# Kernel optimization log

Measured on AMD Instinct MI355X. Metric: run time of the kernel, lower is better.

The kernel has to match this reference:

```python
import jax, jax.numpy as jnp
import numpy as np

B, T, D_MODEL = 2, 2048, 2048
N_HEADS, N_KV, HEAD_DIM = 16, 8, 128
ROPE_BASE = 10000.0
LAMBDA_INIT = 0.2  # 0.8 - 0.6*exp(-0.3*0), layer_depth=0


def rms_norm(x):
    eps = jnp.finfo(x.dtype).eps
    return x * jax.lax.rsqrt(jnp.mean(x * x, axis=-1, keepdims=True) + eps)


def rope_cos_sin(seq_len, dim):
    inv_freq = 1.0 / (ROPE_BASE ** (np.arange(0, dim, 2, dtype=np.float32) / dim))
    t = np.arange(seq_len, dtype=np.float32)
    freqs = np.outer(t, inv_freq)  # [T, dim/2]
    # original caches cos/sin in bfloat16
    cos = jnp.asarray(np.cos(freqs)).astype(jnp.bfloat16).astype(jnp.float32)
    sin = jnp.asarray(np.sin(freqs)).astype(jnp.bfloat16).astype(jnp.float32)
    return cos[None, :, None, :], sin[None, :, None, :]


def apply_rotary(x, cos, sin):
    d = x.shape[-1] // 2
    x1, x2 = x[..., :d], x[..., d:]
    return jnp.concatenate([x1 * cos + x2 * sin, -x1 * sin + x2 * cos], axis=-1)


def causal_attn(q, k, v):
    # q: [B,T,H,Dq], k: [B,S,H,Dq], v: [B,S,H,Dv]
    scale = 1.0 / np.sqrt(q.shape[-1]).astype(np.float32)
    s = jnp.einsum('bthd,bshd->bhts', q, k) * scale
    mask = jnp.tril(jnp.ones((q.shape[1], k.shape[1]), dtype=bool))
    s = jnp.where(mask, s, -jnp.inf)
    p = jax.nn.softmax(s, axis=-1)
    return jnp.einsum('bhts,bshe->bthe', p, v)


def diff_attention(x, Wq, Wk, Wv, lambda_q1, lambda_k1, lambda_q2, lambda_k2, softmax_scaler):
    b, t, _ = x.shape
    q = (x @ Wq.T).reshape(b, t, N_HEADS, HEAD_DIM)
    k = (x @ Wk.T).reshape(b, t, N_KV, HEAD_DIM)
    v = (x @ Wv.T).reshape(b, t, N_KV // 2, 2 * HEAD_DIM)
    cos, sin = rope_cos_sin(t, HEAD_DIM)
    q, k = rms_norm(q), rms_norm(k)
    q, k = apply_rotary(q, cos, sin), apply_rotary(k, cos, sin)
    k = k.reshape(b, t, 2, N_KV // 2, HEAD_DIM)
    k1, k2 = k[:, :, 0], k[:, :, 1]
    # scalable softmax: q *= scaler_h * log(position)
    pos = jnp.arange(1, t + 1, dtype=jnp.float32).reshape(1, t, 1, 1)
    q = softmax_scaler.reshape(1, 1, -1, 1) * jnp.log(pos) * q
    q = q.reshape(b, t, 2, N_HEADS // 2, HEAD_DIM)
    q1, q2 = q[:, :, 0], q[:, :, 1]
    rep = N_HEADS // N_KV  # GQA repeat
    k1 = jnp.repeat(k1, rep, axis=2)
    k2 = jnp.repeat(k2, rep, axis=2)
    vr = jnp.repeat(v, rep, axis=2)
    y1 = causal_attn(q1, k1, vr)
    y2 = causal_attn(q2, k2, vr)
    lam1 = jnp.exp(jnp.sum(lambda_q1 * lambda_k1))
    lam2 = jnp.exp(jnp.sum(lambda_q2 * lambda_k2))
    lam = lam1 - lam2 + LAMBDA_INIT
    return y1 - lam * y2  # [B,T,N_HEADS//2, 2*HEAD_DIM]


def setup_inputs() -> dict:
    key = jax.random.key(0)
    ks = jax.random.split(key, 8)
    return {
        'x': jax.random.normal(ks[0], (B, T, D_MODEL), dtype=jnp.float32),
        'Wq': jax.random.normal(ks[1], (N_HEADS * HEAD_DIM, D_MODEL), dtype=jnp.float32) * 0.02,
        'Wk': jax.random.normal(ks[2], (N_KV * HEAD_DIM, D_MODEL), dtype=jnp.float32) * 0.02,
        'Wv': jax.random.normal(ks[3], (N_KV * HEAD_DIM, D_MODEL), dtype=jnp.float32) * 0.02,
        'lambda_q1': jax.random.normal(ks[4], (HEAD_DIM // 2,), dtype=jnp.float32) * 0.1,
        'lambda_k1': jax.random.normal(ks[5], (HEAD_DIM // 2,), dtype=jnp.float32) * 0.1,
        'lambda_q2': jax.random.normal(ks[6], (HEAD_DIM // 2,), dtype=jnp.float32) * 0.1,
        'lambda_k2': jax.random.normal(ks[7], (HEAD_DIM // 2,), dtype=jnp.float32) * 0.1,
        'softmax_scaler': jnp.ones((N_HEADS,), dtype=jnp.float32),
    }


def reference(x, Wq, Wk, Wv, lambda_q1, lambda_k1, lambda_q2, lambda_k2, softmax_scaler):
    return diff_attention(x, Wq, Wk, Wv, lambda_q1, lambda_k1, lambda_q2, lambda_k2, softmax_scaler)
```

## Files before the change

kernel.cpp:

```cpp
#include <hip/hip_runtime.h>

#define T_SEQ 2048
#define DMODEL 2048
#define BSZ 2
#define MROWS (BSZ * T_SEQ)
#define NQKV 4096
#define NEG_BIG (-1e30f)

typedef __attribute__((ext_vector_type(8))) _Float16 half8;
typedef __attribute__((ext_vector_type(4))) _Float16 half4;
typedef __attribute__((ext_vector_type(4))) float f32x4;

typedef const __attribute__((address_space(1))) unsigned int* gas_ptr;
typedef __attribute__((address_space(3))) unsigned int* las_ptr;
#define GLD16(g, l) __builtin_amdgcn_global_load_lds((gas_ptr)(g), (las_ptr)(l), 16, 0, 0)

__device__ __forceinline__ unsigned short f2bf(float f) {
  unsigned u = __float_as_uint(f);
  unsigned r = (u + 0x7fffu + ((u >> 16) & 1u)) >> 16;
  return (unsigned short)r;
}
__device__ __forceinline__ float bf2f(unsigned short h) {
  return __uint_as_float(((unsigned)h) << 16);
}

__global__ void build_rope(float* __restrict__ cosT, float* __restrict__ sinT) {
  int t = blockIdx.x;
  int i = threadIdx.x;
  float inv = (float)pow(10000.0, -((double)(2 * i)) / 128.0);
  float fr = (float)t * inv;
  cosT[t * 64 + i] = bf2f(f2bf(cosf(fr)));
  sinT[t * 64 + i] = bf2f(f2bf(sinf(fr)));
}

__global__ __launch_bounds__(256) void cvt_x(const float* __restrict__ x,
                                             _Float16* __restrict__ xh) {
  size_t o = ((size_t)blockIdx.x * 256 + threadIdx.x) * 8;
  float4 v0 = *(const float4*)(x + o);
  float4 v1 = *(const float4*)(x + o + 4);
  half8 r;
  r[0] = (_Float16)v0.x; r[1] = (_Float16)v0.y; r[2] = (_Float16)v0.z; r[3] = (_Float16)v0.w;
  r[4] = (_Float16)v1.x; r[5] = (_Float16)v1.y; r[6] = (_Float16)v1.z; r[7] = (_Float16)v1.w;
  *(half8*)(xh + o) = r;
}

__global__ __launch_bounds__(256) void cvt_w(const float* __restrict__ Wq,
                                             const float* __restrict__ Wk,
                                             const float* __restrict__ Wv,
                                             _Float16* __restrict__ wh) {
  size_t o = ((size_t)blockIdx.x * 256 + threadIdx.x) * 8;
  int row = (int)(o >> 11), col = (int)(o & 2047);
  const float* src = (row < 2048) ? (Wq + (size_t)row * 2048)
                    : (row < 3072) ? (Wk + (size_t)(row - 2048) * 2048)
                                   : (Wv + (size_t)(row - 3072) * 2048);
  float4 v0 = *(const float4*)(src + col);
  float4 v1 = *(const float4*)(src + col + 4);
  half8 r;
  r[0] = (_Float16)v0.x; r[1] = (_Float16)v0.y; r[2] = (_Float16)v0.z; r[3] = (_Float16)v0.w;
  r[4] = (_Float16)v1.x; r[5] = (_Float16)v1.y; r[6] = (_Float16)v1.z; r[7] = (_Float16)v1.w;
  *(half8*)(wh + o) = r;
}

__global__ __launch_bounds__(256) void gemm_nt(const _Float16* __restrict__ A,
                                               const _Float16* __restrict__ Bw,
                                               _Float16* __restrict__ C) {
  const int K = DMODEL, N = NQKV;
  __shared__ _Float16 At[128 * 40];
  __shared__ _Float16 Bt[128 * 40];
  int tid = threadIdx.x;
  int lane = tid & 63, w = tid >> 6;
  int wm = w >> 1, wn = w & 1;
  int l15 = lane & 15, quad = lane >> 4;
  int bm = blockIdx.y, bn = blockIdx.x;

  f32x4 acc[4][4];
#pragma unroll
  for (int i = 0; i < 4; i++)
#pragma unroll
    for (int j = 0; j < 4; j++) acc[i][j] = (f32x4){0.f, 0.f, 0.f, 0.f};

  for (int k0 = 0; k0 < K; k0 += 32) {
    __syncthreads();
#pragma unroll
    for (int i = 0; i < 2; i++) {
      int idx = i * 256 + tid;
      int r = idx >> 2, c = idx & 3;
      *(half8*)&At[r * 40 + c * 8] =
          *(const half8*)(A + (size_t)(bm * 128 + r) * K + k0 + c * 8);
      *(half8*)&Bt[r * 40 + c * 8] =
          *(const half8*)(Bw + (size_t)(bn * 128 + r) * K + k0 + c * 8);
    }
    __syncthreads();
    half8 af[4], bfr[4];
#pragma unroll
    for (int i = 0; i < 4; i++)
      af[i] = *(const half8*)&At[(wm * 64 + i * 16 + l15) * 40 + quad * 8];
#pragma unroll
    for (int j = 0; j < 4; j++)
      bfr[j] = *(const half8*)&Bt[(wn * 64 + j * 16 + l15) * 40 + quad * 8];
#pragma unroll
    for (int i = 0; i < 4; i++)
#pragma unroll
      for (int j = 0; j < 4; j++)
        acc[i][j] = __builtin_amdgcn_mfma_f32_16x16x32_f16(af[i], bfr[j], acc[i][j], 0, 0, 0);
  }
#pragma unroll
  for (int i = 0; i < 4; i++)
#pragma unroll
    for (int j = 0; j < 4; j++)
#pragma unroll
      for (int r = 0; r < 4; r++) {
        int row = bm * 128 + wm * 64 + i * 16 + quad * 4 + r;
        int col = bn * 128 + wn * 64 + j * 16 + l15;
        C[(size_t)row * N + col] = (_Float16)acc[i][j][r];
      }
}

__global__ __launch_bounds__(128) void postproc(_Float16* __restrict__ qkv,
                                                const float* __restrict__ cosT,
                                                const float* __restrict__ sinT,
                                                _Float16* __restrict__ kp) {
  int t = blockIdx.x, h = blockIdx.y, b = blockIdx.z;
  int d = threadIdx.x;
  int col = (h < 16) ? (h * 128 + d) : (2048 + (h - 16) * 128 + d);
  size_t idx = ((size_t)(b * T_SEQ + t)) * NQKV + col;
  float v = (float)qkv[idx];
  float ss = v * v;
#pragma unroll
  for (int m = 1; m < 64; m <<= 1) ss += __shfl_xor(ss, m, 64);
  __shared__ float sred[2];
  __shared__ float xs[128];
  if ((threadIdx.x & 63) == 0) sred[threadIdx.x >> 6] = ss;
  __syncthreads();
  float total = sred[0] + sred[1];
  float rn = rsqrtf(total * (1.0f / 128.0f) + 1.1920929e-7f);
  float xn = v * rn;
  xs[d] = xn;
  __syncthreads();
  float o;
  if (d < 64) {
    float c = cosT[t * 64 + d], s = sinT[t * 64 + d];
    o = xn * c + xs[d + 64] * s;
  } else {
    float c = cosT[t * 64 + d - 64], s = sinT[t * 64 + d - 64];
    o = -xs[d - 64] * s + xn * c;
  }
  if (h < 16)
    qkv[idx] = (_Float16)o;
  else
    kp[(((size_t)(b * 8 + (h - 16))) * T_SEQ + t) * 128 + d] = (_Float16)o;
}

__global__ void transpose_v(const _Float16* __restrict__ qkv,
                            _Float16* __restrict__ vt) {
  __shared__ _Float16 tile[32][33];
  int t0 = blockIdx.x * 32, d0 = blockIdx.y * 32;
  int bz = blockIdx.z;
  int b = bz >> 2, vh = bz & 3;
  int tx = threadIdx.x, ty = threadIdx.y;
#pragma unroll
  for (int i = 0; i < 4; i++) {
    int t = t0 + ty + i * 8;
    tile[ty + i * 8][tx] = qkv[((size_t)(b * T_SEQ + t)) * NQKV + 3072 + vh * 256 + d0 + tx];
  }
  __syncthreads();
#pragma unroll
  for (int i = 0; i < 4; i++) {
    int d = d0 + ty + i * 8;
    vt[(((size_t)(b * 4 + vh)) * 256 + d) * T_SEQ + t0 + tx] = tile[tx][ty + i * 8];
  }
}

__global__ __launch_bounds__(256) void attn(const _Float16* __restrict__ qkv,
                                            const _Float16* __restrict__ kp,
                                            const _Float16* __restrict__ vt,
                                            const float* __restrict__ scaler,
                                            float* __restrict__ y1out,
                                            _Float16* __restrict__ y2out) {
  __shared__ __align__(16) char Ks[2][64 * 256];
  __shared__ __align__(16) char Vs[2][128 * 128];
  __shared__ _Float16 Pt[4 * 16 * 72];

  int tid = threadIdx.x, lane = tid & 63, w = tid >> 6;
  int l15 = lane & 15, quad = lane >> 4;
  int bx = blockIdx.x, hh = blockIdx.y, z = blockIdx.z;
  int b = z >> 1, br = z & 1;
  int qh = br * 8 + hh;
  int kh = br * 4 + (hh >> 1);
  int vh = hh >> 1;

  const char* kbase_b = (const char*)(kp + ((size_t)(b * 8 + kh)) * T_SEQ * 128);
  const char* vbase_b = (const char*)(vt + ((size_t)(b * 4 + vh)) * 256 * T_SEQ);
  _Float16* pw = &Pt[w * 16 * 72];
  float sc = scaler[qh] * 0.08838834764831844f;

  int krow_l = lane >> 4;
  int kpc    = (lane & 15) << 4;
  int vrow_l = lane >> 3;
  int vpc    = (lane & 7) << 4;

  auto stageK = [&](int kt1) {
    int ksr = kt1 * 64;
    char* dstb = Ks[kt1 & 1];
#pragma unroll
    for (int c2 = 0; c2 < 4; c2++) {
      int c = w * 4 + c2;
      int row = c * 4 + krow_l;
      const char* src = kbase_b + (((size_t)(ksr + row)) << 8) + (kpc ^ ((row & 7) << 4));
      GLD16(src, dstb + (c << 10));
    }
  };
  auto stageV = [&](int kt1) {
    int ksb = kt1 * 128;
#pragma unroll
    for (int h = 0; h < 2; h++)
#pragma unroll
      for (int c2 = 0; c2 < 4; c2++) {
        int c = w * 4 + c2;
        int d = h * 128 + c * 8 + vrow_l;
        const char* src = vbase_b + (size_t)d * (T_SEQ * 2) + ksb + (vpc ^ (vrow_l << 4));
        GLD16(src, Vs[h] + (c << 10));
      }
  };

  for (int half = 0; half < 2; half++) {
    int qt = half ? (31 - bx) : bx;
    int t0 = qt * 64;
    int tg = t0 + w * 16 + l15;

    const _Float16* qbase = qkv + ((size_t)(b * T_SEQ + tg)) * NQKV + qh * 128;
    half8 qf[4];
#pragma unroll
    for (int kc = 0; kc < 4; kc++)
      qf[kc] = *(const half8*)(qbase + kc * 32 + quad * 8);

    stageK(0);
    stageV(0);
    __builtin_amdgcn_sched_barrier(0);

    float mrow = NEG_BIG, lrow = 0.f;
    float rowscale = sc * logf((float)(tg + 1));
    f32x4 acc[16];
#pragma unroll
    for (int nb = 0; nb < 16; nb++) acc[nb] = (f32x4){0.f, 0.f, 0.f, 0.f};

    for (int kt = 0; kt <= qt; kt++) {
      int ks = kt * 64;
      bool notlast = (kt < qt);

      asm volatile("s_waitcnt vmcnt(8)" ::: "memory");
      __builtin_amdgcn_s_barrier();
      __builtin_amdgcn_sched_barrier(0);
      if (notlast) stageK(kt + 1);

      const char* kbuf = Ks[kt & 1];
      f32x4 sv[4];
#pragma unroll
      for (int j = 0; j < 4; j++) {
        int row = j * 16 + l15;
        int sw = (row & 7) << 4;
        const char* kr = kbuf + (row << 8);
        half8 kf0 = *(const half8*)(kr + (((quad << 4) + 0) ^ sw));
        half8 kf1 = *(const half8*)(kr + (((quad << 4) + 64) ^ sw));
        half8 kf2 = *(const half8*)(kr + (((quad << 4) + 128) ^ sw));
        half8 kf3 = *(const half8*)(kr + (((quad << 4) + 192) ^ sw));
        f32x4 a = (f32x4){0.f, 0.f, 0.f, 0.f};
        a = __builtin_amdgcn_mfma_f32_16x16x32_f16(kf0, qf[0], a, 0, 0, 0);
        a = __builtin_amdgcn_mfma_f32_16x16x32_f16(kf1, qf[1], a, 0, 0, 0);
        a = __builtin_amdgcn_mfma_f32_16x16x32_f16(kf2, qf[2], a, 0, 0, 0);
        a = __builtin_amdgcn_mfma_f32_16x16x32_f16(kf3, qf[3], a, 0, 0, 0);
        sv[j] = a;
      }

      bool diag = (kt == qt);
      float s_r[16];
      float mx = NEG_BIG;
#pragma unroll
      for (int j = 0; j < 4; j++)
#pragma unroll
        for (int r = 0; r < 4; r++) {
          float s = sv[j][r] * rowscale;
          if (diag) {
            int kg = ks + j * 16 + quad * 4 + r;
            if (kg > tg) s = NEG_BIG;
          }
          s_r[j * 4 + r] = s;
          mx = fmaxf(mx, s);
        }
      mx = fmaxf(mx, __shfl_xor(mx, 16, 64));
      mx = fmaxf(mx, __shfl_xor(mx, 32, 64));
      float mnew = fmaxf(mrow, mx);
      float alpha = __expf(mrow - mnew);
      float p[16];
      float rs = 0.f;
#pragma unroll
      for (int i = 0; i < 16; i++) {
        p[i] = __expf(s_r[i] - mnew);
        rs += p[i];
      }
      rs += __shfl_xor(rs, 16, 64);
      rs += __shfl_xor(rs, 32, 64);
      lrow = lrow * alpha + rs;
      mrow = mnew;
      float at[4];
#pragma unroll
      for (int r = 0; r < 4; r++) at[r] = __shfl(alpha, quad * 20 + r, 64);
#pragma unroll
      for (int nb = 0; nb < 16; nb++)
#pragma unroll
        for (int r = 0; r < 4; r++) acc[nb][r] *= at[r];

#pragma unroll
      for (int j = 0; j < 4; j++) {
        half4 pk;
        pk[0] = (_Float16)p[j * 4 + 0];
        pk[1] = (_Float16)p[j * 4 + 1];
        pk[2] = (_Float16)p[j * 4 + 2];
        pk[3] = (_Float16)p[j * 4 + 3];
        *(half4*)&pw[l15 * 72 + j * 16 + quad * 4] = pk;
      }
      half8 pf0 = *(const half8*)&pw[l15 * 72 + quad * 8];
      half8 pf1 = *(const half8*)&pw[l15 * 72 + 32 + quad * 8];

      if (notlast)
        asm volatile("s_waitcnt vmcnt(4)" ::: "memory");
      else
        asm volatile("s_waitcnt vmcnt(0)" ::: "memory");
      __builtin_amdgcn_s_barrier();
      __builtin_amdgcn_sched_barrier(0);

#pragma unroll
      for (int h = 0; h < 2; h++) {
#pragma unroll
        for (int nbl = 0; nbl < 8; nbl++) {
          int row = nbl * 16 + l15;
          int sw = (row & 7) << 4;
          const char* vr = Vs[h] + (row << 7);
          half8 vf0 = *(const half8*)(vr + (((quad << 4) + 0) ^ sw));
          half8 vf1 = *(const half8*)(vr + (((quad << 4) + 64) ^ sw));
          int nb = h * 8 + nbl;
          acc[nb] = __builtin_amdgcn_mfma_f32_16x16x32_f16(pf0, vf0, acc[nb], 0, 0, 0);
          acc[nb] = __builtin_amdgcn_mfma_f32_16x16x32_f16(pf1, vf1, acc[nb], 0, 0, 0);
        }
      }

      asm volatile("s_waitcnt lgkmcnt(0)" ::: "memory");
      __builtin_amdgcn_s_barrier();
      __builtin_amdgcn_sched_barrier(0);
      if (notlast) stageV(kt + 1);
    }

    float linv = 1.0f / lrow;
    float lt[4];
#pragma unroll
    for (int r = 0; r < 4; r++) lt[r] = __shfl(linv, quad * 20 + r, 64);
#pragma unroll
    for (int r = 0; r < 4; r++) {
      int tr = t0 + w * 16 + quad * 4 + r;
      size_t base = ((size_t)(b * T_SEQ + tr)) * 2048 + hh * 256;
      if (br) {
#pragma unroll
        for (int nb = 0; nb < 16; nb++)
          y2out[base + nb * 16 + l15] = (_Float16)(acc[nb][r] * lt[r]);
      } else {
#pragma unroll
        for (int nb = 0; nb < 16; nb++)
          y1out[base + nb * 16 + l15] = acc[nb][r] * lt[r];
      }
    }
  }
}

__global__ __launch_bounds__(256) void combine(float* __restrict__ out,
                                               const _Float16* __restrict__ y2,
                                               const float* __restrict__ lq1,
                                               const float* __restrict__ lk1,
                                               const float* __restrict__ lq2,
                                               const float* __restrict__ lk2) {
  int lane = threadIdx.x & 63;
  float a = lq1[lane] * lk1[lane];
  float bb = lq2[lane] * lk2[lane];
#pragma unroll
  for (int m = 1; m < 64; m <<= 1) {
    a += __shfl_xor(a, m, 64);
    bb += __shfl_xor(bb, m, 64);
  }
  float lam = expf(a) - expf(bb) + 0.2f;

  size_t o = ((size_t)blockIdx.x * 256 + threadIdx.x) * 8;
  half8 yv = *(const half8*)(y2 + o);
  float4 a0 = *(float4*)(out + o);
  float4 a1 = *(float4*)(out + o + 4);
  a0.x -= lam * (float)yv[0];
  a0.y -= lam * (float)yv[1];
  a0.z -= lam * (float)yv[2];
  a0.w -= lam * (float)yv[3];
  a1.x -= lam * (float)yv[4];
  a1.y -= lam * (float)yv[5];
  a1.z -= lam * (float)yv[6];
  a1.w -= lam * (float)yv[7];
  *(float4*)(out + o) = a0;
  *(float4*)(out + o + 4) = a1;
}

extern "C" void kernel_launch(void* const* d_in, const int* in_sizes, int n_in,
                              void* d_out, int out_size, void* d_ws, size_t ws_size,
                              hipStream_t stream) {
  const float* x   = (const float*)d_in[0];
  const float* Wq  = (const float*)d_in[1];
  const float* Wk  = (const float*)d_in[2];
  const float* Wv  = (const float*)d_in[3];
  const float* lq1 = (const float*)d_in[4];
  const float* lk1 = (const float*)d_in[5];
  const float* lq2 = (const float*)d_in[6];
  const float* lk2 = (const float*)d_in[7];
  const float* scaler = (const float*)d_in[8];
  float* out = (float*)d_out;

  char* W = (char*)d_ws;
  _Float16* xh   = (_Float16*)(W + 0);
  _Float16* wh   = (_Float16*)(W + 16777216);
  _Float16* qkvh = (_Float16*)(W + 33554432);
  _Float16* kph  = (_Float16*)(W + 0);
  _Float16* vtb  = (_Float16*)(W + 8388608);
  _Float16* y2h  = (_Float16*)(W + 16777216);
  float* cosT    = out;
  float* sinT    = out + 131072;

  build_rope<<<T_SEQ, 64, 0, stream>>>(cosT, sinT);
  cvt_x<<<4096, 256, 0, stream>>>(x, xh);
  cvt_w<<<4096, 256, 0, stream>>>(Wq, Wk, Wv, wh);
  gemm_nt<<<dim3(NQKV / 128, MROWS / 128), 256, 0, stream>>>(xh, wh, qkvh);
  postproc<<<dim3(T_SEQ, 24, BSZ), 128, 0, stream>>>(qkvh, cosT, sinT, kph);
  transpose_v<<<dim3(T_SEQ / 32, 256 / 32, BSZ * 4), dim3(32, 8), 0, stream>>>(qkvh, vtb);
  attn<<<dim3(16, 8, BSZ * 2), 256, 0, stream>>>(qkvh, kph, vtb, scaler, out, y2h);
  combine<<<4096, 256, 0, stream>>>(out, y2h, lq1, lk1, lq2, lk2);
}
```

Measured before the change: 363.9 us.

## Double-buffer QKV GEMM with direct global-to-LDS loads and merge conversion kernels

Rewrites the QKV projection GEMM main loop to use a K-tile of 64 halves, double-buffered in LDS and filled via global_load_lds with an XOR swizzle, waiting on vmcnt so the next tile's loads overlap the current tile's MFMAs. This removes register staging and the padded shared layout, and halves the number of k-iterations. It also fuses the x and weight fp32-to-fp16 conversion kernels into one launch. Shared memory use rises to 64KB per block, which may reduce occupancy.

New measurement: 330.1 us. -9.3%, faster.

```diff
diff --git a/kernel.cpp b/kernel.cpp
--- a/kernel.cpp
+++ b/kernel.cpp
@@ -33,77 +33,110 @@
   sinT[t * 64 + i] = bf2f(f2bf(sinf(fr)));
 }
 
-__global__ __launch_bounds__(256) void cvt_x(const float* __restrict__ x,
-                                             _Float16* __restrict__ xh) {
-  size_t o = ((size_t)blockIdx.x * 256 + threadIdx.x) * 8;
-  float4 v0 = *(const float4*)(x + o);
-  float4 v1 = *(const float4*)(x + o + 4);
+__global__ __launch_bounds__(256) void cvt_xw(const float* __restrict__ x,
+                                              const float* __restrict__ Wq,
+                                              const float* __restrict__ Wk,
+                                              const float* __restrict__ Wv,
+                                              _Float16* __restrict__ xh,
+                                              _Float16* __restrict__ wh) {
+  int bid = blockIdx.x;
+  size_t o = ((size_t)(bid & 4095) * 256 + threadIdx.x) * 8;
+  const float* src;
+  _Float16* dst;
+  if (bid < 4096) {
+    src = x + o;
+    dst = xh + o;
+  } else {
+    int row = (int)(o >> 11), col = (int)(o & 2047);
+    src = ((row < 2048) ? (Wq + (size_t)row * 2048)
+          : (row < 3072) ? (Wk + (size_t)(row - 2048) * 2048)
+                         : (Wv + (size_t)(row - 3072) * 2048)) + col;
+    dst = wh + o;
+  }
+  float4 v0 = *(const float4*)(src);
+  float4 v1 = *(const float4*)(src + 4);
   half8 r;
   r[0] = (_Float16)v0.x; r[1] = (_Float16)v0.y; r[2] = (_Float16)v0.z; r[3] = (_Float16)v0.w;
   r[4] = (_Float16)v1.x; r[5] = (_Float16)v1.y; r[6] = (_Float16)v1.z; r[7] = (_Float16)v1.w;
-  *(half8*)(xh + o) = r;
-}
-
-__global__ __launch_bounds__(256) void cvt_w(const float* __restrict__ Wq,
-                                             const float* __restrict__ Wk,
-                                             const float* __restrict__ Wv,
-                                             _Float16* __restrict__ wh) {
-  size_t o = ((size_t)blockIdx.x * 256 + threadIdx.x) * 8;
-  int row = (int)(o >> 11), col = (int)(o & 2047);
-  const float* src = (row < 2048) ? (Wq + (size_t)row * 2048)
-                    : (row < 3072) ? (Wk + (size_t)(row - 2048) * 2048)
-                                   : (Wv + (size_t)(row - 3072) * 2048);
-  float4 v0 = *(const float4*)(src + col);
-  float4 v1 = *(const float4*)(src + col + 4);
-  half8 r;
-  r[0] = (_Float16)v0.x; r[1] = (_Float16)v0.y; r[2] = (_Float16)v0.z; r[3] = (_Float16)v0.w;
-  r[4] = (_Float16)v1.x; r[5] = (_Float16)v1.y; r[6] = (_Float16)v1.z; r[7] = (_Float16)v1.w;
-  *(half8*)(wh + o) = r;
+  *(half8*)(dst) = r;
 }
 
 __global__ __launch_bounds__(256) void gemm_nt(const _Float16* __restrict__ A,
                                                const _Float16* __restrict__ Bw,
                                                _Float16* __restrict__ C) {
   const int K = DMODEL, N = NQKV;
-  __shared__ _Float16 At[128 * 40];
-  __shared__ _Float16 Bt[128 * 40];
+  __shared__ __align__(16) char As[2][128 * 128];
+  __shared__ __align__(16) char Bs[2][128 * 128];
   int tid = threadIdx.x;
   int lane = tid & 63, w = tid >> 6;
   int wm = w >> 1, wn = w & 1;
   int l15 = lane & 15, quad = lane >> 4;
   int bm = blockIdx.y, bn = blockIdx.x;
 
+  const char* Aab = (const char*)(A + (size_t)(bm * 128) * K);
+  const char* Bab = (const char*)(Bw + (size_t)(bn * 128) * K);
+  int srow = lane >> 3;
+  int scol = ((lane & 7) ^ srow) << 4;
+
+  auto stage = [&](int t) {
+    int buf = t & 1;
+    size_t kb = (size_t)t << 7;
+#pragma unroll
+    for (int g = 0; g < 4; g++) {
+      int row = w * 32 + g * 8 + srow;
+      GLD16(Aab + (size_t)row * (K * 2) + kb + scol, &As[buf][w * 4096 + g * 1024]);
+    }
+#pragma unroll
+    for (int g = 0; g < 4; g++) {
+      int row = w * 32 + g * 8 + srow;
+      GLD16(Bab + (size_t)row * (K * 2) + kb + scol, &Bs[buf][w * 4096 + g * 1024]);
+    }
+  };
+
   f32x4 acc[4][4];
 #pragma unroll
   for (int i = 0; i < 4; i++)
 #pragma unroll
     for (int j = 0; j < 4; j++) acc[i][j] = (f32x4){0.f, 0.f, 0.f, 0.f};
 
-  for (int k0 = 0; k0 < K; k0 += 32) {
-    __syncthreads();
-#pragma unroll
-    for (int i = 0; i < 2; i++) {
-      int idx = i * 256 + tid;
-      int r = idx >> 2, c = idx & 3;
-      *(half8*)&At[r * 40 + c * 8] =
-          *(const half8*)(A + (size_t)(bm * 128 + r) * K + k0 + c * 8);
-      *(half8*)&Bt[r * 40 + c * 8] =
-          *(const half8*)(Bw + (size_t)(bn * 128 + r) * K + k0 + c * 8);
-    }
-    __syncthreads();
-    half8 af[4], bfr[4];
-#pragma unroll
-    for (int i = 0; i < 4; i++)
-      af[i] = *(const half8*)&At[(wm * 64 + i * 16 + l15) * 40 + quad * 8];
-#pragma unroll
-    for (int j = 0; j < 4; j++)
-      bfr[j] = *(const half8*)&Bt[(wn * 64 + j * 16 + l15) * 40 + quad * 8];
-#pragma unroll
-    for (int i = 0; i < 4; i++)
-#pragma unroll
-      for (int j = 0; j < 4; j++)
-        acc[i][j] = __builtin_amdgcn_mfma_f32_16x16x32_f16(af[i], bfr[j], acc[i][j], 0, 0, 0);
-  }
+  stage(0);
+  for (int t = 0; t < 32; t++) {
+    if (t < 31) {
+      stage(t + 1);
+      asm volatile("s_waitcnt vmcnt(8)" ::: "memory");
+    } else {
+      asm volatile("s_waitcnt vmcnt(0)" ::: "memory");
+    }
+    __builtin_amdgcn_s_barrier();
+    __builtin_amdgcn_sched_barrier(0);
+
+    const char* ab = As[t & 1];
+    const char* bb = Bs[t & 1];
+#pragma unroll
+    for (int kc = 0; kc < 2; kc++) {
+      half8 af[4], bfr[4];
+#pragma unroll
+      for (int i = 0; i < 4; i++) {
+        int row = wm * 64 + i * 16 + l15;
+        af[i] = *(const half8*)(ab + row * 128 + ((kc * 64 + quad * 16) ^ ((row & 7) << 4)));
+      }
+#pragma unroll
+      for (int j = 0; j < 4; j++) {
+        int row = wn * 64 + j * 16 + l15;
+        bfr[j] = *(const half8*)(bb + row * 128 + ((kc * 64 + quad * 16) ^ ((row & 7) << 4)));
+      }
+#pragma unroll
+      for (int i = 0; i < 4; i++)
+#pragma unroll
+        for (int j = 0; j < 4; j++)
+          acc[i][j] = __builtin_amdgcn_mfma_f32_16x16x32_f16(af[i], bfr[j], acc[i][j], 0, 0, 0);
+    }
+
+    asm volatile("s_waitcnt lgkmcnt(0)" ::: "memory");
+    __builtin_amdgcn_s_barrier();
+    __builtin_amdgcn_sched_barrier(0);
+  }
+
 #pragma unroll
   for (int i = 0; i < 4; i++)
 #pragma unroll
@@ -428,8 +461,7 @@
   float* sinT    = out + 131072;
 
   build_rope<<<T_SEQ, 64, 0, stream>>>(cosT, sinT);
-  cvt_x<<<4096, 256, 0, stream>>>(x, xh);
-  cvt_w<<<4096, 256, 0, stream>>>(Wq, Wk, Wv, wh);
+  cvt_xw<<<8192, 256, 0, stream>>>(x, Wq, Wk, Wv, xh, wh);
   gemm_nt<<<dim3(NQKV / 128, MROWS / 128), 256, 0, stream>>>(xh, wh, qkvh);
   postproc<<<dim3(T_SEQ, 24, BSZ), 128, 0, stream>>>(qkvh, cosT, sinT, kph);
   transpose_v<<<dim3(T_SEQ / 32, 256 / 32, BSZ * 4), dim3(32, 8), 0, stream>>>(qkvh, vtb);
```
